# Kernel tuning notes

Measured on AMD Instinct MI355X. Metric: run time of the kernel, lower is better.

Reference implementation:

```python
import jax, jax.numpy as jnp
import numpy as np

SEQ_LEN = 4096
IN_DIM = 1024
QVK_DIM = 1024


def setup_inputs() -> dict:
    key = jax.random.key(0)
    kx, kw = jax.random.split(key)
    x = jax.random.normal(kx, (SEQ_LEN, IN_DIM), dtype=jnp.float32)
    # glorot-uniform-ish scale for W: limit = sqrt(6/(fan_in+fan_out))
    limit = np.sqrt(6.0 / (IN_DIM + 3 * QVK_DIM)).astype(np.float32)
    W = jax.random.uniform(kw, (IN_DIM, 3 * QVK_DIM), dtype=jnp.float32,
                           minval=-limit, maxval=limit)
    return {"x": x, "W": W}


def reference(x, W):
    seq_len = x.shape[0]
    qvk = x @ W                                   # [S, 3*D]
    # NOTE: original splits as queries, VALS, keys (vals is the middle chunk)
    queries, vals, keys = jnp.split(qvk, 3, axis=1)
    raw = (queries @ keys.T) / jnp.sqrt(jnp.float32(QVK_DIM))  # [S, S]
    # causal mask: strictly-upper-triangular entries -> -inf (same as the
    # original's scatter of -inf at triu_indices(seq_len, 1))
    causal = jnp.tril(jnp.ones((seq_len, seq_len), dtype=bool))
    raw = jnp.where(causal, raw, -jnp.inf)
    weights = jax.nn.softmax(raw, axis=1)
    return weights @ vals                         # [S, D]
```

## Files before the change

kernel.cpp:

```cpp
#include <hip/hip_runtime.h>

#define SEQ 4096
#define KDIM 1024
#define NQKV 3072
#define BK 32

typedef __bf16 bf16x8 __attribute__((ext_vector_type(8)));
typedef float  f32x4  __attribute__((ext_vector_type(4)));

#define WAITV(n) asm volatile("s_waitcnt vmcnt(" #n ")" ::: "memory")
#define BAR()    asm volatile("s_barrier" ::: "memory")

__device__ __forceinline__ unsigned short f2b(float f) {
    unsigned int u = __float_as_uint(f);
    u += 0x7FFFu + ((u >> 16) & 1u);
    return (unsigned short)(u >> 16);
}
__device__ __forceinline__ float b2f(unsigned short h) {
    return __uint_as_float(((unsigned int)h) << 16);
}

__device__ __forceinline__ void gld_lds16(const unsigned short* g, unsigned short* l) {
    __builtin_amdgcn_global_load_lds(
        (const __attribute__((address_space(1))) void*)g,
        (__attribute__((address_space(3))) void*)l, 16, 0, 0);
}

__device__ __forceinline__ void stage_tiles(
    const unsigned short* Ag, int lda, const unsigned short* Bg, int ldb,
    int k0, unsigned short* sA, unsigned short* sB, int wave, int lane)
{
    #pragma unroll
    for (int i = 0; i < 2; ++i) {
        int c = wave * 128 + i * 64 + lane;
        int row = c >> 2, slot = c & 3;
        int p = slot ^ ((row >> 1) & 3);
        gld_lds16(Ag + row * lda + k0 + p * 8, sA + (wave * 2 + i) * 512);
        gld_lds16(Bg + row * ldb + k0 + p * 8, sB + (wave * 2 + i) * 512);
    }
}

__device__ __forceinline__ const unsigned short* frag_addr(
    const unsigned short* s, int row, int quad)
{
    return s + row * 32 + (quad ^ ((row >> 1) & 3)) * 8;
}

__device__ __forceinline__ void compute_tile(
    const unsigned short* sA, const unsigned short* sB, f32x4 acc[4][4],
    int wm, int wn, int lr, int quad)
{
    bf16x8 af[4], bq[4];
    #pragma unroll
    for (int i = 0; i < 4; ++i)
        af[i] = *(const bf16x8*)frag_addr(sA, wm + 16 * i + lr, quad);
    #pragma unroll
    for (int j = 0; j < 4; ++j)
        bq[j] = *(const bf16x8*)frag_addr(sB, wn + 16 * j + lr, quad);
    #pragma unroll
    for (int i = 0; i < 4; ++i)
        #pragma unroll
        for (int j = 0; j < 4; ++j)
            acc[i][j] = __builtin_amdgcn_mfma_f32_16x16x32_bf16(af[i], bq[j], acc[i][j], 0, 0, 0);
}

__device__ __forceinline__ void mfma_pipe(
    const unsigned short* Ag, int lda, const unsigned short* Bg, int ldb,
    int kLen, unsigned short* lds, f32x4 acc[4][4])
{
    const int tid  = threadIdx.x;
    const int wave = tid >> 6, lane = tid & 63;
    const int lr   = lane & 15, quad = lane >> 4;
    const int wm   = (wave >> 1) * 64, wn = (wave & 1) * 64;
    const int niter = kLen >> 5;

    #pragma unroll
    for (int s = 0; s < 3; ++s)
        if (s < niter)
            stage_tiles(Ag, lda, Bg, ldb, s * BK,
                        lds + s * 8192, lds + s * 8192 + 4096, wave, lane);

    #pragma unroll 1
    for (int k = 0; k < niter; ++k) {
        if (k + 2 < niter)      WAITV(8);
        else if (k + 1 < niter) WAITV(4);
        else                    WAITV(0);
        BAR();
        if (k + 3 < niter) {
            const int s = (k + 3) & 3;
            stage_tiles(Ag, lda, Bg, ldb, (k + 3) * BK,
                        lds + s * 8192, lds + s * 8192 + 4096, wave, lane);
        }
        const int c = k & 3;
        compute_tile(lds + c * 8192, lds + c * 8192 + 4096, acc, wm, wn, lr, quad);
    }
}

__device__ __forceinline__ void zero_acc(f32x4 acc[4][4]) {
    const f32x4 z = {0.f, 0.f, 0.f, 0.f};
    #pragma unroll
    for (int i = 0; i < 4; ++i)
        #pragma unroll
        for (int j = 0; j < 4; ++j) acc[i][j] = z;
}

__device__ __forceinline__ void store_rows_bf16(
    f32x4 acc[4][4], unsigned short* Cw, int ld, unsigned short* lw, int lane)
{
    const int lr = lane & 15, quad = lane >> 4;
    #pragma unroll
    for (int i = 0; i < 4; ++i) {
        #pragma unroll
        for (int j = 0; j < 4; ++j)
            #pragma unroll
            for (int r = 0; r < 4; ++r)
                lw[(quad * 4 + r) * 72 + j * 16 + lr] = f2b(acc[i][j][r]);
        #pragma unroll
        for (int t = 0; t < 2; ++t) {
            int chunk = t * 64 + lane;
            int rl = chunk >> 3, c8 = chunk & 7;
            uint4 v = *(const uint4*)(lw + rl * 72 + c8 * 8);
            *(uint4*)(Cw + (16 * i + rl) * ld + c8 * 8) = v;
        }
    }
}

__device__ __forceinline__ void store_cols_bf16(
    f32x4 acc[4][4], unsigned short* Vw, unsigned short* lw, int lane)
{
    const int lr = lane & 15, quad = lane >> 4;
    #pragma unroll
    for (int ip = 0; ip < 2; ++ip) {
        #pragma unroll
        for (int ii = 0; ii < 2; ++ii)
            #pragma unroll
            for (int j = 0; j < 4; ++j)
                #pragma unroll
                for (int r = 0; r < 4; ++r)
                    lw[(j * 16 + lr) * 40 + ii * 16 + quad * 4 + r] = f2b(acc[ip * 2 + ii][j][r]);
        #pragma unroll
        for (int t = 0; t < 4; ++t) {
            int chunk = t * 64 + lane;
            int col = chunk >> 2, c8 = chunk & 3;
            uint4 v = *(const uint4*)(lw + col * 40 + c8 * 8);
            *(uint4*)(Vw + col * SEQ + ip * 32 + c8 * 8) = v;
        }
    }
}

__global__ __launch_bounds__(256) void prep(
    const float* __restrict__ x, unsigned short* __restrict__ Xb,
    const float* __restrict__ W, unsigned short* __restrict__ Wt,
    float4* __restrict__ out, float4* __restrict__ lrow)
{
    __shared__ float tile[32][33];
    const int b = blockIdx.x, tid = threadIdx.x;
    if (b < 4096) {
        int i = (b * 256 + tid) * 4;
        float4 v = *(const float4*)(x + i);
        ushort4 o;
        o.x = f2b(v.x); o.y = f2b(v.y); o.z = f2b(v.z); o.w = f2b(v.w);
        *(ushort4*)(Xb + i) = o;
    } else if (b < 8192) {
        const float4 z = {0.f, 0.f, 0.f, 0.f};
        out[(b - 4096) * 256 + tid] = z;
    } else if (b < 11264) {
        const int bb = b - 8192;
        const int n0 = (bb % 96) * 32, k0 = (bb / 96) * 32;
        const int c = tid & 31, r0 = tid >> 5;
        #pragma unroll
        for (int r = r0; r < 32; r += 8)
            tile[r][c] = W[(k0 + r) * NQKV + n0 + c];
        __syncthreads();
        #pragma unroll
        for (int r = r0; r < 32; r += 8)
            Wt[(n0 + r) * KDIM + k0 + c] = f2b(tile[c][r]);
    } else {
        const float4 z = {0.f, 0.f, 0.f, 0.f};
        #pragma unroll
        for (int k = 0; k < 4; ++k) lrow[tid * 4 + k] = z;
    }
}

__global__ __launch_bounds__(256) void qvk_gemm(
    const unsigned short* __restrict__ Xb, const unsigned short* __restrict__ Wt,
    unsigned short* __restrict__ Qb, unsigned short* __restrict__ Kb,
    unsigned short* __restrict__ Vt)
{
    __shared__ __align__(16) unsigned short lds[32768];
    const int m0 = blockIdx.x * 128;
    const int n0 = blockIdx.y * 128;
    f32x4 acc[4][4];
    zero_acc(acc);
    mfma_pipe(Xb + m0 * KDIM, KDIM, Wt + n0 * KDIM, KDIM, KDIM, lds, acc);
    __syncthreads();

    const int lane = threadIdx.x & 63, wave = threadIdx.x >> 6;
    const int wm = (wave >> 1) * 64, wn = (wave & 1) * 64;
    unsigned short* lw = lds + wave * 2560;
    const int region = n0 >> 10;
    const int nloc = n0 & 1023;
    if (region == 0)
        store_rows_bf16(acc, Qb + (m0 + wm) * KDIM + nloc + wn, KDIM, lw, lane);
    else if (region == 2)
        store_rows_bf16(acc, Kb + (m0 + wm) * KDIM + nloc + wn, KDIM, lw, lane);
    else
        store_cols_bf16(acc, Vt + (nloc + wn) * SEQ + m0 + wm, lw, lane);
}

__global__ __launch_bounds__(256) void score_exp_gemm(
    const unsigned short* __restrict__ Qb, const unsigned short* __restrict__ Kb,
    unsigned short* __restrict__ Sb, float* __restrict__ lrow)
{
    __shared__ __align__(16) unsigned short lds[32768];
    const int bm = blockIdx.x, bn = blockIdx.y;
    if (bn > bm) return;
    const int m0 = bm * 128, n0 = bn * 128;

    f32x4 acc[4][4];
    zero_acc(acc);
    mfma_pipe(Qb + m0 * KDIM, KDIM, Kb + n0 * KDIM, KDIM, KDIM, lds, acc);

    const int lane = threadIdx.x & 63, wave = threadIdx.x >> 6;
    const int lr = lane & 15, quad = lane >> 4;
    const int wm = (wave >> 1) * 64, wn = (wave & 1) * 64;
    #pragma unroll
    for (int i = 0; i < 4; ++i)
        #pragma unroll
        for (int j = 0; j < 4; ++j)
            #pragma unroll
            for (int r = 0; r < 4; ++r) {
                float v = __expf(acc[i][j][r] * 0.03125f);
                if (bm == bn) {
                    int row = wm + 16 * i + quad * 4 + r;
                    int col = wn + 16 * j + lr;
                    if (col > row) v = 0.f;
                }
                acc[i][j][r] = v;
            }
    #pragma unroll
    for (int i = 0; i < 4; ++i)
        #pragma unroll
        for (int r = 0; r < 4; ++r) {
            float s = acc[i][0][r] + acc[i][1][r] + acc[i][2][r] + acc[i][3][r];
            s += __shfl_xor(s, 1, 16);
            s += __shfl_xor(s, 2, 16);
            s += __shfl_xor(s, 4, 16);
            s += __shfl_xor(s, 8, 16);
            if (lr == 0)
                atomicAdd(&lrow[m0 + wm + 16 * i + quad * 4 + r], s);
        }
    __syncthreads();
    store_rows_bf16(acc, Sb + (m0 + wm) * SEQ + n0 + wn, SEQ, lds + wave * 2560, lane);
}

__global__ __launch_bounds__(256) void pv_gemm(
    const unsigned short* __restrict__ Sb, const unsigned short* __restrict__ Vt,
    const float* __restrict__ lrow, float* __restrict__ out)
{
    __shared__ __align__(16) unsigned short lds[32768];
    const int n0 = blockIdx.y * 128;
    const int y = blockIdx.x;
    int m, c;
    if (y < 8)       { m = y;                 c = 0; }
    else if (y < 24) { m = 8 + (y - 8) / 2;   c = (y - 8) % 2; }
    else if (y < 48) { m = 16 + (y - 24) / 3; c = (y - 24) % 3; }
    else             { m = 24 + (y - 48) / 4; c = (y - 48) % 4; }
    const int m0 = m * 128;
    const int kstart = c * 1024;
    const int kend = min((m + 1) * 128, kstart + 1024);
    const int nchunks = (m >> 3) + 1;

    f32x4 acc[4][4];
    zero_acc(acc);
    mfma_pipe(Sb + m0 * SEQ + kstart, SEQ, Vt + n0 * SEQ + kstart, SEQ,
              kend - kstart, lds, acc);

    const int lane = threadIdx.x & 63, wave = threadIdx.x >> 6;
    const int lr = lane & 15, quad = lane >> 4;
    const int wm = (wave >> 1) * 64, wn = (wave & 1) * 64;
    #pragma unroll
    for (int i = 0; i < 4; ++i) {
        const int rbase = m0 + wm + 16 * i + quad * 4;
        const float4 l4 = *(const float4*)(lrow + rbase);
        float inv[4] = {1.0f / l4.x, 1.0f / l4.y, 1.0f / l4.z, 1.0f / l4.w};
        #pragma unroll
        for (int j = 0; j < 4; ++j) {
            const int col = n0 + wn + 16 * j + lr;
            if (nchunks == 1) {
                #pragma unroll
                for (int r = 0; r < 4; ++r)
                    out[(rbase + r) * KDIM + col] = acc[i][j][r] * inv[r];
            } else {
                #pragma unroll
                for (int r = 0; r < 4; ++r)
                    atomicAdd(&out[(rbase + r) * KDIM + col], acc[i][j][r] * inv[r]);
            }
        }
    }
}

extern "C" void kernel_launch(void* const* d_in, const int* in_sizes, int n_in,
                              void* d_out, int out_size, void* d_ws, size_t ws_size,
                              hipStream_t stream) {
    const float* x = (const float*)d_in[0];
    const float* W = (const float*)d_in[1];
    float* out = (float*)d_out;
    char* ws = (char*)d_ws;

    unsigned short* Xb = (unsigned short*)(ws);
    unsigned short* Wt = (unsigned short*)(ws + 8388608);
    unsigned short* Qb = (unsigned short*)(ws + 14680064);
    unsigned short* Kb = (unsigned short*)(ws + 23068672);
    unsigned short* Vt = (unsigned short*)(ws + 31457280);
    unsigned short* Sb = (unsigned short*)(ws + 39845888);
    float*        lrow = (float*)(ws + 73400320);

    prep          <<<11265, 256, 0, stream>>>(x, Xb, W, Wt, (float4*)out, (float4*)lrow);
    qvk_gemm      <<<dim3(SEQ / 128, NQKV / 128), 256, 0, stream>>>(Xb, Wt, Qb, Kb, Vt);
    score_exp_gemm<<<dim3(SEQ / 128, SEQ / 128), 256, 0, stream>>>(Qb, Kb, Sb, lrow);
    pv_gemm       <<<dim3(80, KDIM / 128), 256, 0, stream>>>(Sb, Vt, lrow, out);
}
```

Baseline: 205.5 us.

## Use 3-stage LDS pipeline for QKV and score GEMMs, vectorize W transpose, reorder pv grid

New measurement: 204.5 us. No clear change (-0.5%).

```diff
diff --git a/kernel.cpp b/kernel.cpp
--- a/kernel.cpp
+++ b/kernel.cpp
@@ -15,9 +15,6 @@
     unsigned int u = __float_as_uint(f);
     u += 0x7FFFu + ((u >> 16) & 1u);
     return (unsigned short)(u >> 16);
-}
-__device__ __forceinline__ float b2f(unsigned short h) {
-    return __uint_as_float(((unsigned int)h) << 16);
 }
 
 __device__ __forceinline__ void gld_lds16(const unsigned short* g, unsigned short* l) {
@@ -64,7 +61,38 @@
             acc[i][j] = __builtin_amdgcn_mfma_f32_16x16x32_bf16(af[i], bq[j], acc[i][j], 0, 0, 0);
 }
 
-__device__ __forceinline__ void mfma_pipe(
+__device__ __forceinline__ void mfma_pipe3(
+    const unsigned short* Ag, int lda, const unsigned short* Bg, int ldb,
+    int kLen, unsigned short* lds, f32x4 acc[4][4])
+{
+    const int tid  = threadIdx.x;
+    const int wave = tid >> 6, lane = tid & 63;
+    const int lr   = lane & 15, quad = lane >> 4;
+    const int wm   = (wave >> 1) * 64, wn = (wave & 1) * 64;
+    const int niter = kLen >> 5;
+
+    #pragma unroll
+    for (int s = 0; s < 2; ++s)
+        if (s < niter)
+            stage_tiles(Ag, lda, Bg, ldb, s * BK,
+                        lds + s * 8192, lds + s * 8192 + 4096, wave, lane);
+
+    #pragma unroll 1
+    for (int k = 0; k < niter; ++k) {
+        if (k + 1 < niter) WAITV(4);
+        else               WAITV(0);
+        BAR();
+        if (k + 2 < niter) {
+            const int s = (k + 2) % 3;
+            stage_tiles(Ag, lda, Bg, ldb, (k + 2) * BK,
+                        lds + s * 8192, lds + s * 8192 + 4096, wave, lane);
+        }
+        const int c = k % 3;
+        compute_tile(lds + c * 8192, lds + c * 8192 + 4096, acc, wm, wn, lr, quad);
+    }
+}
+
+__device__ __forceinline__ void mfma_pipe4(
     const unsigned short* Ag, int lda, const unsigned short* Bg, int ldb,
     int kLen, unsigned short* lds, f32x4 acc[4][4])
 {
@@ -172,9 +200,13 @@
         for (int r = r0; r < 32; r += 8)
             tile[r][c] = W[(k0 + r) * NQKV + n0 + c];
         __syncthreads();
-        #pragma unroll
-        for (int r = r0; r < 32; r += 8)
-            Wt[(n0 + r) * KDIM + k0 + c] = f2b(tile[c][r]);
+        const int n = tid >> 3, q = tid & 7;
+        ushort4 o;
+        o.x = f2b(tile[q * 4 + 0][n]);
+        o.y = f2b(tile[q * 4 + 1][n]);
+        o.z = f2b(tile[q * 4 + 2][n]);
+        o.w = f2b(tile[q * 4 + 3][n]);
+        *(ushort4*)(Wt + (n0 + n) * KDIM + k0 + q * 4) = o;
     } else {
         const float4 z = {0.f, 0.f, 0.f, 0.f};
         #pragma unroll
@@ -187,12 +219,12 @@
     unsigned short* __restrict__ Qb, unsigned short* __restrict__ Kb,
     unsigned short* __restrict__ Vt)
 {
-    __shared__ __align__(16) unsigned short lds[32768];
+    __shared__ __align__(16) unsigned short lds[24576];
     const int m0 = blockIdx.x * 128;
     const int n0 = blockIdx.y * 128;
     f32x4 acc[4][4];
     zero_acc(acc);
-    mfma_pipe(Xb + m0 * KDIM, KDIM, Wt + n0 * KDIM, KDIM, KDIM, lds, acc);
+    mfma_pipe3(Xb + m0 * KDIM, KDIM, Wt + n0 * KDIM, KDIM, KDIM, lds, acc);
     __syncthreads();
 
     const int lane = threadIdx.x & 63, wave = threadIdx.x >> 6;
@@ -212,14 +244,14 @@
     const unsigned short* __restrict__ Qb, const unsigned short* __restrict__ Kb,
     unsigned short* __restrict__ Sb, float* __restrict__ lrow)
 {
-    __shared__ __align__(16) unsigned short lds[32768];
+    __shared__ __align__(16) unsigned short lds[24576];
     const int bm = blockIdx.x, bn = blockIdx.y;
     if (bn > bm) return;
     const int m0 = bm * 128, n0 = bn * 128;
 
     f32x4 acc[4][4];
     zero_acc(acc);
-    mfma_pipe(Qb + m0 * KDIM, KDIM, Kb + n0 * KDIM, KDIM, KDIM, lds, acc);
+    mfma_pipe3(Qb + m0 * KDIM, KDIM, Kb + n0 * KDIM, KDIM, KDIM, lds, acc);
 
     const int lane = threadIdx.x & 63, wave = threadIdx.x >> 6;
     const int lr = lane & 15, quad = lane >> 4;
@@ -238,6 +270,8 @@
                 }
                 acc[i][j][r] = v;
             }
+    __syncthreads();
+    store_rows_bf16(acc, Sb + (m0 + wm) * SEQ + n0 + wn, SEQ, lds + wave * 2560, lane);
     #pragma unroll
     for (int i = 0; i < 4; ++i)
         #pragma unroll
@@ -250,8 +284,6 @@
             if (lr == 0)
                 atomicAdd(&lrow[m0 + wm + 16 * i + quad * 4 + r], s);
         }
-    __syncthreads();
-    store_rows_bf16(acc, Sb + (m0 + wm) * SEQ + n0 + wn, SEQ, lds + wave * 2560, lane);
 }
 
 __global__ __launch_bounds__(256) void pv_gemm(
@@ -259,8 +291,8 @@
     const float* __restrict__ lrow, float* __restrict__ out)
 {
     __shared__ __align__(16) unsigned short lds[32768];
-    const int n0 = blockIdx.y * 128;
-    const int y = blockIdx.x;
+    const int n0 = blockIdx.x * 128;
+    const int y = blockIdx.y;
     int m, c;
     if (y < 8)       { m = y;                 c = 0; }
     else if (y < 24) { m = 8 + (y - 8) / 2;   c = (y - 8) % 2; }
@@ -273,8 +305,8 @@
 
     f32x4 acc[4][4];
     zero_acc(acc);
-    mfma_pipe(Sb + m0 * SEQ + kstart, SEQ, Vt + n0 * SEQ + kstart, SEQ,
-              kend - kstart, lds, acc);
+    mfma_pipe4(Sb + m0 * SEQ + kstart, SEQ, Vt + n0 * SEQ + kstart, SEQ,
+               kend - kstart, lds, acc);
 
     const int lane = threadIdx.x & 63, wave = threadIdx.x >> 6;
     const int lr = lane & 15, quad = lane >> 4;
@@ -319,5 +351,5 @@
     prep          <<<11265, 256, 0, stream>>>(x, Xb, W, Wt, (float4*)out, (float4*)lrow);
     qvk_gemm      <<<dim3(SEQ / 128, NQKV / 128), 256, 0, stream>>>(Xb, Wt, Qb, Kb, Vt);
     score_exp_gemm<<<dim3(SEQ / 128, SEQ / 128), 256, 0, stream>>>(Qb, Kb, Sb, lrow);
-    pv_gemm       <<<dim3(80, KDIM / 128), 256, 0, stream>>>(Sb, Vt, lrow, out);
-}
+    pv_gemm       <<<dim3(KDIM / 128, 80), 256, 0, stream>>>(Sb, Vt, lrow, out);
+}
```
